# Kernel tuning notes

Hardware: AMD Instinct MI355X
Metric: run time of the kernel (lower is better)

Reference implementation:

```python
import jax, jax.numpy as jnp
import numpy as np

PRE_HEIGHT = 96
PRE_WIDTH = 128


def setup_inputs() -> dict:
    key = jax.random.key(0)
    B, K, H, W = 32, 64, 96, 128
    x = jax.random.normal(key, (B, K, H, W), dtype=jnp.float32)
    return {"combined_hm_preds": x, "batch_size": B, "num_of_kp": K}


def reference(combined_hm_preds, batch_size, num_of_kp):
    B, K, H, W = combined_hm_preds.shape
    # nn.Softmax() with no dim on a 4D tensor -> softmax over dim=1 (channels)
    map_val_all = jax.nn.softmax(combined_hm_preds, axis=1)
    # zeta[b,k] = sum over spatial of the channel-softmaxed map
    get_zeta = map_val_all.sum(axis=(2, 3))  # [B, K]
    js = jnp.arange(W, dtype=map_val_all.dtype)
    iis = jnp.arange(H, dtype=map_val_all.dtype)
    # per-channel weighted coordinate sums
    Sx = jnp.einsum('bkij,j->bk', map_val_all, js)  # [B, K]
    Sy = jnp.einsum('bkij,i->bk', map_val_all, iis)  # [B, K]
    # faithful to the original: accumulators are never reset across k or b,
    # so each keypoint uses the inclusive cumulative sum in flattened (b,k) order
    cum_x = jnp.cumsum(Sx.reshape(-1)).reshape(B, K)
    cum_y = jnp.cumsum(Sy.reshape(-1)).reshape(B, K)
    kx = jnp.round(cum_x / get_zeta)
    ky = jnp.round(cum_y / get_zeta)
    # out-of-range clamp to the image center, as in the original
    kx = jnp.where((kx > PRE_WIDTH) | (kx < 0), PRE_WIDTH * 0.5, kx)
    ky = jnp.where((ky > PRE_HEIGHT) | (ky < 0), PRE_HEIGHT * 0.5, ky)
    keypoint = jnp.stack([kx, ky], axis=-1)  # [B, K, 2]
    return (map_val_all, keypoint, get_zeta)
```

## Files before the change

kernel.cpp:

```cpp
#include <hip/hip_runtime.h>
#include <math.h>

#define BB 32
#define KK 64
#define HH 96
#define WW 128
#define HW (HH*WW)
#define MAP_SIZE (BB*KK*HW)
#define NBK (BB*KK)

__global__ __launch_bounds__(256) void softmax_k(const float* __restrict__ x,
                                                 float* __restrict__ out) {
    int gid = blockIdx.x * 256 + threadIdx.x;
    int b   = gid / HW;
    int pix = gid - b * HW;
    const float* xp = x   + (size_t)b * KK * HW + pix;
    float*       op = out + (size_t)b * KK * HW + pix;

    float v[KK];
    float mx = -INFINITY;
    #pragma unroll
    for (int k = 0; k < KK; ++k) {
        v[k] = xp[(size_t)k * HW];
        mx = fmaxf(mx, v[k]);
    }
    float den = 0.0f;
    #pragma unroll
    for (int k = 0; k < KK; ++k) {
        v[k] = __expf(v[k] - mx);
        den += v[k];
    }
    float inv = 1.0f / den;
    #pragma unroll
    for (int k = 0; k < KK; ++k) {
        op[(size_t)k * HW] = v[k] * inv;
    }
}

__global__ __launch_bounds__(256) void reduce_k(const float* __restrict__ map,
                                                float* __restrict__ zeta_out,
                                                double* __restrict__ sxyz) {
    int bk = blockIdx.x;
    const float* mp = map + (size_t)bk * HW;
    int t = threadIdx.x;

    double z = 0.0, sx = 0.0, sy = 0.0;
    for (int idx = t; idx < HW; idx += 256) {
        float m = mp[idx];
        int j = idx & (WW - 1);
        int i = idx >> 7;
        z  += (double)m;
        sx += (double)m * (double)j;
        sy += (double)m * (double)i;
    }
    for (int off = 32; off > 0; off >>= 1) {
        z  += __shfl_down(z,  off, 64);
        sx += __shfl_down(sx, off, 64);
        sy += __shfl_down(sy, off, 64);
    }
    __shared__ double sz[4], ssx[4], ssy[4];
    int lane = t & 63, wid = t >> 6;
    if (lane == 0) { sz[wid] = z; ssx[wid] = sx; ssy[wid] = sy; }
    __syncthreads();
    if (t == 0) {
        double Z  = sz[0]  + sz[1]  + sz[2]  + sz[3];
        double SX = ssx[0] + ssx[1] + ssx[2] + ssx[3];
        double SY = ssy[0] + ssy[1] + ssy[2] + ssy[3];
        zeta_out[bk]    = (float)Z;
        sxyz[bk*3 + 0]  = SX;
        sxyz[bk*3 + 1]  = SY;
        sxyz[bk*3 + 2]  = Z;
    }
}

__global__ __launch_bounds__(256) void keypoint_k(const double* __restrict__ sxyz,
                                                  float* __restrict__ kp) {
    const int PT = NBK / 256;
    int t = threadIdx.x;
    int lane = t & 63, wid = t >> 6;

    double vx[PT], vy[PT];
    double cx = 0.0, cy = 0.0;
    #pragma unroll
    for (int e = 0; e < PT; ++e) {
        int idx = t * PT + e;
        cx += sxyz[idx*3 + 0]; vx[e] = cx;
        cy += sxyz[idx*3 + 1]; vy[e] = cy;
    }
    double tx = cx, ty = cy;
    for (int off = 1; off < 64; off <<= 1) {
        double ax = __shfl_up(tx, off, 64);
        double ay = __shfl_up(ty, off, 64);
        if (lane >= off) { tx += ax; ty += ay; }
    }
    __shared__ double wxs[4], wys[4];
    if (lane == 63) { wxs[wid] = tx; wys[wid] = ty; }
    __syncthreads();
    double offx = tx - cx, offy = ty - cy;
    for (int w2 = 0; w2 < wid; ++w2) { offx += wxs[w2]; offy += wys[w2]; }

    #pragma unroll
    for (int e = 0; e < PT; ++e) {
        int idx = t * PT + e;
        double z  = sxyz[idx*3 + 2];
        double kx = rint((vx[e] + offx) / z);
        double ky = rint((vy[e] + offy) / z);
        float fkx = (float)kx, fky = (float)ky;
        if (fkx > 128.0f || fkx < 0.0f) fkx = 64.0f;
        if (fky > 96.0f  || fky < 0.0f) fky = 48.0f;
        kp[idx*2 + 0] = fkx;
        kp[idx*2 + 1] = fky;
    }
}

extern "C" void kernel_launch(void* const* d_in, const int* in_sizes, int n_in,
                              void* d_out, int out_size, void* d_ws, size_t ws_size,
                              hipStream_t stream) {
    const float* x = (const float*)d_in[0];
    float* out  = (float*)d_out;
    float* map  = out;
    float* kp   = out + MAP_SIZE;
    float* zeta = out + MAP_SIZE + NBK * 2;
    double* sxyz = (double*)d_ws;

    softmax_k <<< (BB * HW) / 256, 256, 0, stream >>> (x, map);
    reduce_k  <<< NBK,             256, 0, stream >>> (map, zeta, sxyz);
    keypoint_k<<< 1,               256, 0, stream >>> (sxyz, kp);
}
```

Measured before the change: 215.3 us.

## Split softmax into denominator pass and fused map-write plus spatial reduction

A first pass now computes only the per-pixel reciprocal softmax denominator into workspace, using float4 loads. A second per-(b,k) kernel recomputes exp from the input, writes the normalised map and reduces zeta, Sx and Sy in the same pass. This removes the separate pass that re-read the whole map for the reduction and widens memory accesses. In exchange the input is read twice and exp is computed twice. The max subtraction is also dropped, so large logits could overflow exp.

Result: faster. 198.0 us (-8.0%).

```diff
diff --git a/kernel.cpp b/kernel.cpp
--- a/kernel.cpp
+++ b/kernel.cpp
@@ -9,49 +9,58 @@
 #define MAP_SIZE (BB*KK*HW)
 #define NBK (BB*KK)
 
-__global__ __launch_bounds__(256) void softmax_k(const float* __restrict__ x,
-                                                 float* __restrict__ out) {
+__global__ __launch_bounds__(256) void den_k(const float* __restrict__ x,
+                                             float* __restrict__ inv_den) {
     int gid = blockIdx.x * 256 + threadIdx.x;
-    int b   = gid / HW;
-    int pix = gid - b * HW;
-    const float* xp = x   + (size_t)b * KK * HW + pix;
-    float*       op = out + (size_t)b * KK * HW + pix;
+    int b   = gid / (HW / 4);
+    int p4  = gid - b * (HW / 4);
+    const float4* xp = (const float4*)(x + (size_t)b * KK * HW) + p4;
 
-    float v[KK];
-    float mx = -INFINITY;
+    float4 s = {0.f, 0.f, 0.f, 0.f};
     #pragma unroll
     for (int k = 0; k < KK; ++k) {
-        v[k] = xp[(size_t)k * HW];
-        mx = fmaxf(mx, v[k]);
+        float4 v = xp[(size_t)k * (HW / 4)];
+        s.x += __expf(v.x);
+        s.y += __expf(v.y);
+        s.z += __expf(v.z);
+        s.w += __expf(v.w);
     }
-    float den = 0.0f;
-    #pragma unroll
-    for (int k = 0; k < KK; ++k) {
-        v[k] = __expf(v[k] - mx);
-        den += v[k];
-    }
-    float inv = 1.0f / den;
-    #pragma unroll
-    for (int k = 0; k < KK; ++k) {
-        op[(size_t)k * HW] = v[k] * inv;
-    }
+    float4 r = {1.f / s.x, 1.f / s.y, 1.f / s.z, 1.f / s.w};
+    ((float4*)inv_den)[gid] = r;
 }
 
-__global__ __launch_bounds__(256) void reduce_k(const float* __restrict__ map,
-                                                float* __restrict__ zeta_out,
-                                                double* __restrict__ sxyz) {
+__global__ __launch_bounds__(256) void map_reduce_k(const float* __restrict__ x,
+                                                    const float* __restrict__ inv_den,
+                                                    float* __restrict__ out,
+                                                    float* __restrict__ zeta,
+                                                    double* __restrict__ sxyz) {
     int bk = blockIdx.x;
-    const float* mp = map + (size_t)bk * HW;
+    int b  = bk >> 6;
+    const float4* xp = (const float4*)(x        + (size_t)bk * HW);
+    const float4* ip = (const float4*)(inv_den  + (size_t)b  * HW);
+    float4*       op = (float4*)      (out      + (size_t)bk * HW);
     int t = threadIdx.x;
 
     double z = 0.0, sx = 0.0, sy = 0.0;
-    for (int idx = t; idx < HW; idx += 256) {
-        float m = mp[idx];
-        int j = idx & (WW - 1);
-        int i = idx >> 7;
-        z  += (double)m;
-        sx += (double)m * (double)j;
-        sy += (double)m * (double)i;
+    #pragma unroll
+    for (int it = 0; it < 12; ++it) {
+        int idx = it * 256 + t;
+        float4 v   = xp[idx];
+        float4 inv = ip[idx];
+        float4 m;
+        m.x = __expf(v.x) * inv.x;
+        m.y = __expf(v.y) * inv.y;
+        m.z = __expf(v.z) * inv.z;
+        m.w = __expf(v.w) * inv.w;
+        op[idx] = m;
+        int j0 = (idx & 31) * 4;
+        int i  = idx >> 5;
+        float qs = m.x + m.y + m.z + m.w;
+        float qx = m.x * (float)j0 + m.y * (float)(j0 + 1)
+                 + m.z * (float)(j0 + 2) + m.w * (float)(j0 + 3);
+        z  += (double)qs;
+        sx += (double)qx;
+        sy += (double)i * (double)qs;
     }
     for (int off = 32; off > 0; off >>= 1) {
         z  += __shfl_down(z,  off, 64);
@@ -66,10 +75,10 @@
         double Z  = sz[0]  + sz[1]  + sz[2]  + sz[3];
         double SX = ssx[0] + ssx[1] + ssx[2] + ssx[3];
         double SY = ssy[0] + ssy[1] + ssy[2] + ssy[3];
-        zeta_out[bk]    = (float)Z;
-        sxyz[bk*3 + 0]  = SX;
-        sxyz[bk*3 + 1]  = SY;
-        sxyz[bk*3 + 2]  = Z;
+        sxyz[bk * 3 + 0] = SX;
+        sxyz[bk * 3 + 1] = SY;
+        sxyz[bk * 3 + 2] = Z;
+        zeta[bk] = (float)Z;
     }
 }
 
@@ -84,8 +93,8 @@
     #pragma unroll
     for (int e = 0; e < PT; ++e) {
         int idx = t * PT + e;
-        cx += sxyz[idx*3 + 0]; vx[e] = cx;
-        cy += sxyz[idx*3 + 1]; vy[e] = cy;
+        cx += sxyz[idx * 3 + 0]; vx[e] = cx;
+        cy += sxyz[idx * 3 + 1]; vy[e] = cy;
     }
     double tx = cx, ty = cy;
     for (int off = 1; off < 64; off <<= 1) {
@@ -102,14 +111,14 @@
     #pragma unroll
     for (int e = 0; e < PT; ++e) {
         int idx = t * PT + e;
-        double z  = sxyz[idx*3 + 2];
-        double kx = rint((vx[e] + offx) / z);
-        double ky = rint((vy[e] + offy) / z);
+        double zz = sxyz[idx * 3 + 2];
+        double kx = rint((vx[e] + offx) / zz);
+        double ky = rint((vy[e] + offy) / zz);
         float fkx = (float)kx, fky = (float)ky;
         if (fkx > 128.0f || fkx < 0.0f) fkx = 64.0f;
         if (fky > 96.0f  || fky < 0.0f) fky = 48.0f;
-        kp[idx*2 + 0] = fkx;
-        kp[idx*2 + 1] = fky;
+        kp[idx * 2 + 0] = fkx;
+        kp[idx * 2 + 1] = fky;
     }
 }
 
@@ -121,9 +130,11 @@
     float* map  = out;
     float* kp   = out + MAP_SIZE;
     float* zeta = out + MAP_SIZE + NBK * 2;
+
     double* sxyz = (double*)d_ws;
+    float*  inv  = (float*)((char*)d_ws + NBK * 3 * sizeof(double) + 256);
 
-    softmax_k <<< (BB * HW) / 256, 256, 0, stream >>> (x, map);
-    reduce_k  <<< NBK,             256, 0, stream >>> (map, zeta, sxyz);
-    keypoint_k<<< 1,               256, 0, stream >>> (sxyz, kp);
+    den_k       <<< (BB * HW / 4) / 256, 256, 0, stream >>> (x, inv);
+    map_reduce_k<<< NBK,                 256, 0, stream >>> (x, inv, map, zeta, sxyz);
+    keypoint_k  <<< 1,                   256, 0, stream >>> (sxyz, kp);
 }
```
